# Performance work log

Hardware: AMD Instinct MI355X
Metric: run time of the kernel (lower is better)

## Reference

```python
import jax, jax.numpy as jnp
import numpy as np

K_MAX = 64      # config.k_max
N_HASH = 8      # LSH hash bits per table


def setup_inputs() -> dict:
    key = jax.random.key(0)
    kq, kk, kw = jax.random.split(key, 3)
    B, L, D = 4, 2048, 64
    query = jax.random.normal(kq, (B, L, D), dtype=jnp.float32)
    key_t = jax.random.normal(kk, (B, L, D), dtype=jnp.float32)
    W = jax.random.normal(kw, (D, N_HASH), dtype=jnp.float32)  # LSH projection
    return {"query": query, "key": key_t, "W": W, "head_idx": 0}


def _hash_code(x, W):
    # binary_quantize then LSH hash: sign bits of random projection, packed to one int code
    x_bin = jnp.where(x > 0, 1.0, 0.0)                      # [B,L,D]
    bits = (jnp.einsum('bld,dh->blh', x_bin, W) > 0)        # [B,L,H] bool
    weights = (2 ** jnp.arange(N_HASH, dtype=jnp.int32))    # pack bits -> bucket id
    return jnp.sum(bits.astype(jnp.int32) * weights, axis=-1)  # [B,L] int32


def reference(query, key, W, head_idx):
    B, L, _ = query.shape
    q_code = _hash_code(query, W)   # [B,L]
    k_code = _hash_code(key, W)     # [B,L]
    # hash-equality match matrix [B, Lq, Lk] (== .all(dim=2) on hash bits)
    matches = q_code[:, :, None] == k_code[:, None, :]
    idx = jnp.arange(L, dtype=jnp.int32)
    # non-matches get sentinel L so the k_max smallest indices are the first matches
    cand_keys = jnp.where(matches, idx[None, None, :], L)   # [B,L,L]
    neg_top, _ = jax.lax.top_k(-cand_keys, K_MAX)           # k_max smallest indices
    cand = -neg_top                                          # ascending first-match order
    return jnp.where(cand == L, -1, cand).astype(jnp.int64)  # [B,L,k_max], -1 padded
```

## Files before the change

### kernel.cpp

```cpp
#include <hip/hip_runtime.h>

#define D 64
#define H 8
#define LSEQ 2048
#define KMAX 64
#define NCODES 256

__global__ void __launch_bounds__(256)
code_kernel(const float* __restrict__ query,
            const float* __restrict__ key,
            const float* __restrict__ W,
            int* __restrict__ q_code,
            int* __restrict__ k_code,
            int n_pos) {
    __shared__ float Ws[D * H];
    for (int i = threadIdx.x; i < D * H; i += blockDim.x) Ws[i] = W[i];
    __syncthreads();

    int t = blockIdx.x * blockDim.x + threadIdx.x;
    if (t >= 2 * n_pos) return;

    const float* xp = (t < n_pos) ? (query + (size_t)t * D)
                                  : (key + (size_t)(t - n_pos) * D);
    float4 s0 = {0.f, 0.f, 0.f, 0.f};
    float4 s1 = {0.f, 0.f, 0.f, 0.f};

    for (int d4 = 0; d4 < D / 4; ++d4) {
        float4 xv = ((const float4*)xp)[d4];
        const float* x4 = (const float*)&xv;
#pragma unroll
        for (int k = 0; k < 4; ++k) {
            if (x4[k] > 0.0f) {
                int d = d4 * 4 + k;
                float4 w0 = *(const float4*)&Ws[d * H + 0];
                float4 w1 = *(const float4*)&Ws[d * H + 4];
                s0.x += w0.x; s0.y += w0.y; s0.z += w0.z; s0.w += w0.w;
                s1.x += w1.x; s1.y += w1.y; s1.z += w1.z; s1.w += w1.w;
            }
        }
    }
    int c = 0;
    c |= (s0.x > 0.0f) ? 1   : 0;
    c |= (s0.y > 0.0f) ? 2   : 0;
    c |= (s0.z > 0.0f) ? 4   : 0;
    c |= (s0.w > 0.0f) ? 8   : 0;
    c |= (s1.x > 0.0f) ? 16  : 0;
    c |= (s1.y > 0.0f) ? 32  : 0;
    c |= (s1.z > 0.0f) ? 64  : 0;
    c |= (s1.w > 0.0f) ? 128 : 0;

    if (t < n_pos) q_code[t] = c;
    else           k_code[t - n_pos] = c;
}

__global__ void __launch_bounds__(64)
bucket_ballot_kernel(const int* __restrict__ k_code,
                     int* __restrict__ bucket) {
    __shared__ int row[KMAX];
    int c = blockIdx.x & (NCODES - 1);
    int b = blockIdx.x >> 8;
    int lane = threadIdx.x;

    const int* kc = k_code + (size_t)b * LSEQ;
    row[lane] = -1;

    unsigned long long lt_mask = (lane == 63) ? 0x7FFFFFFFFFFFFFFFull
                                              : ((1ull << lane) - 1ull);
    int base = 0;
    for (int i = 0; i < LSEQ / 64; ++i) {
        int idx = i * 64 + lane;
        int ci = kc[idx];
        unsigned long long mask = __ballot(ci == c);
        if (ci == c) {
            int rank = base + __popcll(mask & lt_mask);
            if (rank < KMAX) row[rank] = idx;
        }
        base += __popcll(mask);
        if (base >= KMAX) break;
    }
    __syncthreads();
    bucket[((size_t)b * NCODES + c) * KMAX + lane] = row[lane];
}

__global__ void __launch_bounds__(256)
emit_kernel(const int* __restrict__ q_code,
            const int* __restrict__ bucket,
            int* __restrict__ out, int total) {
    int t = blockIdx.x * blockDim.x + threadIdx.x;
    if (t >= total) return;
    int q = t >> 6;
    int j = t & (KMAX - 1);
    int b = q >> 11;
    int c = q_code[q];
    out[t] = bucket[((size_t)(b * NCODES + c)) * KMAX + j];
}

extern "C" void kernel_launch(void* const* d_in, const int* in_sizes, int n_in,
                              void* d_out, int out_size, void* d_ws, size_t ws_size,
                              hipStream_t stream) {
    const float* query = (const float*)d_in[0];
    const float* key   = (const float*)d_in[1];
    const float* W     = (const float*)d_in[2];

    int n_pos = in_sizes[0] / D;
    int B     = n_pos / LSEQ;

    int* q_code = (int*)d_ws;
    int* k_code = q_code + n_pos;
    int* bucket = k_code + n_pos;

    {
        int total = 2 * n_pos;
        code_kernel<<<(total + 255) / 256, 256, 0, stream>>>(query, key, W,
                                                             q_code, k_code, n_pos);
    }
    {
        bucket_ballot_kernel<<<B * NCODES, 64, 0, stream>>>(k_code, bucket);
    }
    {
        int total = out_size;
        emit_kernel<<<(total + 255) / 256, 256, 0, stream>>>(q_code, bucket,
                                                             (int*)d_out, total);
    }
}
```

Measured before the change: 80.47 us.

## Fuse bucket scan and emit into per-query wave scan kernel

Replaces the per-(batch,code) bucket construction kernel and the separate gather/emit kernel with one kernel where each wave scans the key codes for its own query's hash code and writes the first 64 matches directly to the output. This removes a kernel launch and the intermediate bucket buffer round trip. In exchange, the scan work grows because buckets are rebuilt per query rather than shared among queries with the same code.

```diff
diff --git a/kernel.cpp b/kernel.cpp
--- a/kernel.cpp
+++ b/kernel.cpp
@@ -53,15 +53,19 @@
     else           k_code[t - n_pos] = c;
 }
 
-__global__ void __launch_bounds__(64)
-bucket_ballot_kernel(const int* __restrict__ k_code,
-                     int* __restrict__ bucket) {
-    __shared__ int row[KMAX];
-    int c = blockIdx.x & (NCODES - 1);
-    int b = blockIdx.x >> 8;
-    int lane = threadIdx.x;
+__global__ void __launch_bounds__(256)
+scan_emit_kernel(const int* __restrict__ q_code,
+                 const int* __restrict__ k_code,
+                 int* __restrict__ out) {
+    __shared__ int rows[4][KMAX];
+    int wave = threadIdx.x >> 6;
+    int lane = threadIdx.x & 63;
+    int q = blockIdx.x * 4 + wave;
+    int b = q >> 11;
 
+    int c = q_code[q];
     const int* kc = k_code + (size_t)b * LSEQ;
+    int* row = rows[wave];
     row[lane] = -1;
 
     unsigned long long lt_mask = (lane == 63) ? 0x7FFFFFFFFFFFFFFFull
@@ -78,21 +82,7 @@
         base += __popcll(mask);
         if (base >= KMAX) break;
     }
-    __syncthreads();
-    bucket[((size_t)b * NCODES + c) * KMAX + lane] = row[lane];
-}
-
-__global__ void __launch_bounds__(256)
-emit_kernel(const int* __restrict__ q_code,
-            const int* __restrict__ bucket,
-            int* __restrict__ out, int total) {
-    int t = blockIdx.x * blockDim.x + threadIdx.x;
-    if (t >= total) return;
-    int q = t >> 6;
-    int j = t & (KMAX - 1);
-    int b = q >> 11;
-    int c = q_code[q];
-    out[t] = bucket[((size_t)(b * NCODES + c)) * KMAX + j];
+    out[(size_t)q * KMAX + lane] = row[lane];
 }
 
 extern "C" void kernel_launch(void* const* d_in, const int* in_sizes, int n_in,
@@ -103,11 +93,10 @@
     const float* W     = (const float*)d_in[2];
 
     int n_pos = in_sizes[0] / D;
-    int B     = n_pos / LSEQ;
+    (void)ws_size;
 
     int* q_code = (int*)d_ws;
     int* k_code = q_code + n_pos;
-    int* bucket = k_code + n_pos;
 
     {
         int total = 2 * n_pos;
@@ -115,11 +104,7 @@
                                                              q_code, k_code, n_pos);
     }
     {
-        bucket_ballot_kernel<<<B * NCODES, 64, 0, stream>>>(k_code, bucket);
-    }
-    {
-        int total = out_size;
-        emit_kernel<<<(total + 255) / 256, 256, 0, stream>>>(q_code, bucket,
-                                                             (int*)d_out, total);
+        scan_emit_kernel<<<n_pos / 4, 256, 0, stream>>>(q_code, k_code,
+                                                        (int*)d_out);
     }
 }
```

Result: faster. 78.52 us (-2.4%).
